# Optimization experiments

Measured on AMD Instinct MI355X. Metric: run time of the kernel, lower is better.

The kernel has to match this reference:

```python
import jax, jax.numpy as jnp
import numpy as np

B, S = 4, 1024
VD, TD, HD = 1024, 768, 2048
NH = 16
HDIM = HD // NH
SCALE = HDIM ** -0.5
THRESH = 2.0 / 3.0


def bitnet_linear(x, w, b):
    # BitNet b1.58 eval-mode: per-tensor abs-mean scale, clamp, ternarize, dense matmul
    scale = jnp.clip(jnp.mean(jnp.abs(w)), 1e-5, 1000.0)
    wn = jnp.clip(w / scale, -10.0, 10.0)
    q = jnp.where(wn > THRESH, 1.0, jnp.where(wn < -THRESH, -1.0, 0.0))
    return x @ (q * scale).T + b


def layernorm(x, g, b, eps=1e-5):
    mu = jnp.mean(x, axis=-1, keepdims=True)
    var = jnp.mean(jnp.square(x - mu), axis=-1, keepdims=True)
    return (x - mu) * jax.lax.rsqrt(var + eps) * g + b


def setup_inputs() -> dict:
    key = jax.random.key(0)
    ks = jax.random.split(key, 8)
    return {
        "vision_features": jax.random.normal(ks[0], (B, VD), jnp.float32),
        "text_features": jax.random.normal(ks[1], (B, S, TD), jnp.float32),
        "text_mask": jnp.ones((B, S), dtype=bool),
        "w_vision_proj": jax.random.normal(ks[2], (HD, VD), jnp.float32),
        "b_vision_proj": jnp.zeros((HD,), jnp.float32),
        "w_text_proj": jax.random.normal(ks[3], (HD, TD), jnp.float32),
        "b_text_proj": jnp.zeros((HD,), jnp.float32),
        "w_text_qkv": jax.random.normal(ks[4], (3 * HD, HD), jnp.float32),
        "b_text_qkv": jnp.zeros((3 * HD,), jnp.float32),
        "ln_text_g": jnp.ones((HD,), jnp.float32),
        "ln_text_b": jnp.zeros((HD,), jnp.float32),
        "w_out": jax.random.normal(ks[5], (HD, HD), jnp.float32),
        "b_out": jnp.zeros((HD,), jnp.float32),
        "ln_cross_g": jnp.ones((HD,), jnp.float32),
        "ln_cross_b": jnp.zeros((HD,), jnp.float32),
    }


def reference(vision_features, text_features, text_mask,
              w_vision_proj, b_vision_proj, w_text_proj, b_text_proj,
              w_text_qkv, b_text_qkv, ln_text_g, ln_text_b,
              w_out, b_out, ln_cross_g, ln_cross_b):
    # projections into shared hidden space (BitNet ternary linears)
    vp = bitnet_linear(vision_features, w_vision_proj, b_vision_proj)        # [B, HD]
    tp = bitnet_linear(text_features, w_text_proj, b_text_proj)              # [B, S, HD]

    # --- text self-attention (no rel-pos bias: the rel-pos branch raises and is swallowed) ---
    tn = layernorm(tp, ln_text_g, ln_text_b)
    qkv = bitnet_linear(tn, w_text_qkv, b_text_qkv)                          # [B, S, 3*HD]
    qkv = qkv.reshape(B, S, 3, NH, HDIM).transpose(2, 0, 3, 1, 4)            # [3, B, H, S, hd]
    tq, tk, tv = qkv[0], qkv[1], qkv[2]
    attn = jnp.einsum('bhqd,bhkd->bhqk', tq, tk) * SCALE                     # [B, H, S, S]
    attn = jnp.where(text_mask[:, None, None, :], attn, -1e9)
    attn = jax.nn.softmax(attn, axis=-1)
    text_self = jnp.einsum('bhqk,bhkd->bhqd', attn, tv)
    text_self = text_self.transpose(0, 2, 1, 3).reshape(B, S, HD)
    text_self = tp + text_self                                               # residual (dropout=id in eval)

    # --- image-to-text attention ---
    # original repeats the single vision query over seq then means the (identical)
    # outputs; mathematically equal to a single-query attention.
    vq = vp.reshape(B, NH, 1, HDIM)                                          # [B, H, 1, hd]
    tk2 = text_self.reshape(B, S, NH, HDIM).transpose(0, 2, 1, 3)            # [B, H, S, hd]
    i2t = jnp.einsum('bhqd,bhkd->bhqk', vq, tk2) * SCALE                     # [B, H, 1, S]
    i2t = jnp.where(text_mask[:, None, None, :], i2t, -1e9)
    i2t = jax.nn.softmax(i2t, axis=-1)
    i2t_out = jnp.einsum('bhqk,bhkd->bhqd', i2t, tk2).reshape(B, HD)         # [B, HD]

    # --- text-to-image attention (single kv "token" per head -> softmax over size-1 axis) ---
    tq2 = text_self.reshape(B, S, NH, HDIM).transpose(0, 2, 1, 3)            # [B, H, S, hd]
    vk = vp.reshape(B, NH, 1, HDIM)                                          # [B, H, 1, hd]
    t2i = jnp.einsum('bhqd,bhkd->bhqk', tq2, vk) * SCALE                     # [B, H, S, 1]
    t2i = jax.nn.softmax(t2i, axis=-1)                                       # all ones (size-1 axis)
    t2i_out = jnp.einsum('bhqk,bhkd->bhqd', t2i, vk)                         # [B, H, S, hd]
    t2i_out = t2i_out.transpose(0, 2, 1, 3).reshape(B, S, HD)

    # --- fusion: shared BitNet output projection + cross norm (inferred continuation) ---
    fused_vision = layernorm(vp + bitnet_linear(i2t_out, w_out, b_out), ln_cross_g, ln_cross_b)
    fused_text = layernorm(text_self + bitnet_linear(t2i_out, w_out, b_out), ln_cross_g, ln_cross_b)
    return fused_vision, fused_text
```

## Files before the change

### kernel.cpp

```cpp
#include <hip/hip_runtime.h>


typedef unsigned short u16;
typedef unsigned int   u32;
typedef __attribute__((ext_vector_type(4))) float f32x4;
typedef __attribute__((ext_vector_type(8))) short short8;
typedef _Float16 half8 __attribute__((ext_vector_type(8)));

__device__ __forceinline__ u16 f2h(float x) {
    _Float16 h = (_Float16)x;
    return __builtin_bit_cast(u16, h);
}
__device__ __forceinline__ f32x4 mfmah(short8 a, short8 b, f32x4 c) {
    return __builtin_amdgcn_mfma_f32_16x16x32_f16(
        __builtin_bit_cast(half8, a), __builtin_bit_cast(half8, b), c, 0, 0, 0);
}
__device__ __forceinline__ void gload16(const void* g, void* l) {
    __builtin_amdgcn_global_load_lds((const __attribute__((address_space(1))) u32*)g,
                                     (__attribute__((address_space(3))) u32*)l, 16, 0, 0);
}

__device__ __forceinline__ float blockReduceSum256(float v, float* red) {
#pragma unroll
    for (int o = 32; o; o >>= 1) v += __shfl_down(v, o);
    int lane = threadIdx.x & 63, w = threadIdx.x >> 6;
    __syncthreads();
    if (lane == 0) red[w] = v;
    __syncthreads();
    return red[0] + red[1] + red[2] + red[3];
}

__global__ __launch_bounds__(256) void k_absmean4(const float* __restrict__ w0, const float* __restrict__ w1,
                                                  const float* __restrict__ w2, const float* __restrict__ w3,
                                                  int n40, int n41, int n42, int n43,
                                                  double* __restrict__ part) {
    int slot = blockIdx.x >> 8, b = blockIdx.x & 255;
    const float* w = (slot == 0) ? w0 : (slot == 1) ? w1 : (slot == 2) ? w2 : w3;
    int n4 = (slot == 0) ? n40 : (slot == 1) ? n41 : (slot == 2) ? n42 : n43;
    const float4* w4 = (const float4*)w;
    double s = 0.0;
    for (int i = b * 256 + threadIdx.x; i < n4; i += 65536) {
        float4 v = w4[i];
        s += (double)fabsf(v.x) + (double)fabsf(v.y) + (double)fabsf(v.z) + (double)fabsf(v.w);
    }
#pragma unroll
    for (int o = 32; o; o >>= 1) s += __shfl_down(s, o);
    __shared__ double p4[4];
    int lane = threadIdx.x & 63, w_ = threadIdx.x >> 6;
    if (lane == 0) p4[w_] = s;
    __syncthreads();
    if (threadIdx.x == 0) part[slot * 256 + b] = p4[0] + p4[1] + p4[2] + p4[3];
}

__global__ void k_finalize(const double* __restrict__ part, float* __restrict__ scf) {
    int w = threadIdx.x >> 6, lane = threadIdx.x & 63;
    double s = 0.0;
    for (int j = lane; j < 256; j += 64) s += part[w * 256 + j];
#pragma unroll
    for (int o = 32; o; o >>= 1) s += __shfl_down(s, o);
    if (lane == 0) {
        const double ns[4] = {2097152.0, 1572864.0, 12582912.0, 4194304.0};
        float v = (float)(s / ns[w]);
        v = fminf(fmaxf(v, 1e-5f), 1000.0f);
        scf[w] = v;
    }
}

__global__ __launch_bounds__(256) void k_quant(const float* __restrict__ w, u32* __restrict__ qd,
                                               int n2, const float* __restrict__ scf, int slot) {
    float s = scf[slot];
    const float th = 2.0f / 3.0f;
    for (int i = blockIdx.x * blockDim.x + threadIdx.x; i < n2; i += gridDim.x * blockDim.x) {
        float2 v = ((const float2*)w)[i];
        float wn0 = v.x / s, wn1 = v.y / s;
        u32 q0 = (wn0 > th) ? 0x3C00u : ((wn0 < -th) ? 0xBC00u : 0u);
        u32 q1 = (wn1 > th) ? 0x3C00u : ((wn1 < -th) ? 0xBC00u : 0u);
        qd[i] = q0 | (q1 << 16);
    }
}

__global__ __launch_bounds__(256) void k_tofp16(const float* __restrict__ x, u32* __restrict__ xs, int n2) {
    for (int i = blockIdx.x * blockDim.x + threadIdx.x; i < n2; i += gridDim.x * blockDim.x) {
        float2 v = ((const float2*)x)[i];
        xs[i] = (u32)f2h(v.x) | (((u32)f2h(v.y)) << 16);
    }
}

__global__ __launch_bounds__(256) void k_gemm(const u16* __restrict__ A, const u16* __restrict__ Bw,
                                              int K, int N, int NB_N,
                                              const float* __restrict__ scf, int slot,
                                              const float* __restrict__ bias,
                                              float* Cf, u16* Cp, int epi) {
    __shared__ __align__(16) u16 ldsA[2][128 * 64];
    __shared__ __align__(16) u16 ldsB[2][128 * 64];
    int m0 = (blockIdx.x / NB_N) * 128;
    int n0 = (blockIdx.x % NB_N) * 128;
    int t = threadIdx.x, lane = t & 63, w = t >> 6;
    int wm = (w >> 1) * 64, wn = (w & 1) * 64;
    f32x4 acc[4][4];
#pragma unroll
    for (int i = 0; i < 4; i++)
#pragma unroll
        for (int j = 0; j < 4; j++) acc[i][j] = (f32x4)(0.0f);

    auto STAGE = [&](int buf, int k0) {
#pragma unroll
        for (int i = 0; i < 4; i++) {
            int c = i * 256 + t;
            int row = c & 127, kg = c >> 7;
            const u16* ga = A + (size_t)(m0 + row) * K + (k0 + kg * 8);
            const u16* gb = Bw + (size_t)(n0 + row) * K + (k0 + kg * 8);
            int db = (i * 256 + w * 64) * 8;
            gload16(ga, ldsA[buf] + db);
            gload16(gb, ldsB[buf] + db);
        }
    };
    auto COMPUTE = [&](int buf) {
#pragma unroll
        for (int kk = 0; kk < 64; kk += 32) {
            int kg4 = (kk >> 3) + (lane >> 4);
            short8 av[4], bv[4];
#pragma unroll
            for (int mi = 0; mi < 4; mi++)
                av[mi] = *(const short8*)(ldsA[buf] + (size_t)(kg4 * 128 + wm + mi * 16 + (lane & 15)) * 8);
#pragma unroll
            for (int ni = 0; ni < 4; ni++)
                bv[ni] = *(const short8*)(ldsB[buf] + (size_t)(kg4 * 128 + wn + ni * 16 + (lane & 15)) * 8);
#pragma unroll
            for (int mi = 0; mi < 4; mi++)
#pragma unroll
                for (int ni = 0; ni < 4; ni++)
                    acc[mi][ni] = mfmah(av[mi], bv[ni], acc[mi][ni]);
        }
    };

    STAGE(0, 0);
    __syncthreads();
    int cur = 0;
    for (int k0 = 64; k0 < K; k0 += 64) {
        STAGE(cur ^ 1, k0);
        COMPUTE(cur);
        __syncthreads();
        cur ^= 1;
    }
    COMPUTE(cur);

    float s = scf[slot];
#pragma unroll
    for (int ni = 0; ni < 4; ni++) {
        int col = n0 + wn + ni * 16 + (lane & 15);
        float bv = bias[col];
#pragma unroll
        for (int mi = 0; mi < 4; mi++) {
            int rb = m0 + wm + mi * 16 + ((lane >> 4) << 2);
#pragma unroll
            for (int j = 0; j < 4; j++) {
                float y = acc[mi][ni][j] * s + bv;
                if (epi == 0) {
                    Cf[(size_t)(rb + j) * N + col] = y;
                } else {
                    Cp[(size_t)(rb + j) * N + col] = f2h(y);
                }
            }
        }
    }
}

__global__ __launch_bounds__(256) void k_vp(const float* __restrict__ vf, const float* __restrict__ w,
                                            const float* __restrict__ bias, const float* __restrict__ scf,
                                            float* __restrict__ vp) {
    __shared__ float xl[4096];
    int t = threadIdx.x;
#pragma unroll
    for (int i = 0; i < 16; i++) xl[t + i * 256] = vf[t + i * 256];
    __syncthreads();
    int lane = t & 63;
    int n = blockIdx.x * 4 + (t >> 6);
    float s = scf[0];
    const float th = 2.0f / 3.0f;
    float a0 = 0, a1 = 0, a2 = 0, a3 = 0;
    const float* wr = w + (size_t)n * 1024;
    for (int k = lane; k < 1024; k += 64) {
        float wn = wr[k] / s;
        float q = (wn > th) ? 1.0f : ((wn < -th) ? -1.0f : 0.0f);
        a0 += xl[k] * q; a1 += xl[1024 + k] * q; a2 += xl[2048 + k] * q; a3 += xl[3072 + k] * q;
    }
#pragma unroll
    for (int o = 32; o; o >>= 1) {
        a0 += __shfl_down(a0, o); a1 += __shfl_down(a1, o);
        a2 += __shfl_down(a2, o); a3 += __shfl_down(a3, o);
    }
    if (lane == 0) {
        float bv = bias[n];
        vp[n] = a0 * s + bv; vp[2048 + n] = a1 * s + bv;
        vp[4096 + n] = a2 * s + bv; vp[6144 + n] = a3 * s + bv;
    }
}

__global__ __launch_bounds__(256) void k_ln1(const float* __restrict__ x, const float* __restrict__ g,
                                             const float* __restrict__ b, u16* __restrict__ tn) {
    __shared__ float red[4];
    int r = blockIdx.x, t = threadIdx.x;
    const float* xr = x + (size_t)r * 2048;
    float v[8]; float s = 0;
#pragma unroll
    for (int i = 0; i < 8; i++) { v[i] = xr[t + i * 256]; s += v[i]; }
    s = blockReduceSum256(s, red);
    float mu = s * (1.0f / 2048.0f);
    float s2 = 0;
#pragma unroll
    for (int i = 0; i < 8; i++) { float d = v[i] - mu; s2 += d * d; }
    s2 = blockReduceSum256(s2, red);
    float rstd = 1.0f / sqrtf(s2 * (1.0f / 2048.0f) + 1e-5f);
#pragma unroll
    for (int i = 0; i < 8; i++) {
        int c = t + i * 256;
        float y = (v[i] - mu) * rstd * g[c] + b[c];
        tn[(size_t)r * 2048 + c] = f2h(y);
    }
}

__global__ __launch_bounds__(256) void k_attn(const u16* __restrict__ qkv, float* ts) {
    __shared__ __align__(16) u16 kp[8192];
    __shared__ __align__(16) u16 vt[128 * 72];
    int t = threadIdx.x, lane = t & 63, w = t >> 6;
    int bh = blockIdx.x >> 4, qb = blockIdx.x & 15;
    int b = bh >> 4, h = bh & 15;
    int rowbase = b * 1024;
    int q0 = qb * 64 + w * 16;
    u16* pl = kp + (size_t)w * 16 * 72;

    short8 qh[4];
    {
        int r = rowbase + q0 + (lane & 15);
        const u16* qp = qkv + (size_t)r * 6144 + h * 128 + (lane >> 4) * 8;
#pragma unroll
        for (int c4 = 0; c4 < 4; c4++) qh[c4] = *(const short8*)(qp + c4 * 32);
    }
    float m[4], ld[4];
#pragma unroll
    for (int j = 0; j < 4; j++) { m[j] = -1e30f; ld[j] = 0.0f; }
    f32x4 po[8];
#pragma unroll
    for (int nt = 0; nt < 8; nt++) po[nt] = (f32x4)(0.0f);
    const float SC = 0.08838834764831845f;

    for (int kt = 0; kt < 16; kt++) {
        __syncthreads();
#pragma unroll
        for (int i = 0; i < 4; i++) {
            int c = i * 256 + t;
            int sl = c & 63, dg = c >> 6;
            const u16* gk = qkv + (size_t)(rowbase + kt * 64 + sl) * 6144 + (2048 + h * 128 + dg * 8);
            gload16(gk, kp + (size_t)(i * 256 + w * 64) * 8);
        }
#pragma unroll
        for (int i = 0; i < 4; i++) {
            int c = i * 256 + t;
            int sl = c & 63, dg = c >> 6;
            const u16* gv = qkv + (size_t)(rowbase + kt * 64 + sl) * 6144 + (4096 + h * 128 + dg * 8);
            short8 vv = *(const short8*)gv;
#pragma unroll
            for (int j = 0; j < 8; j++) vt[(size_t)(dg * 8 + j) * 72 + sl] = (u16)vv[j];
        }
        __syncthreads();

        f32x4 sacc[4];
#pragma unroll
        for (int nt = 0; nt < 4; nt++) sacc[nt] = (f32x4)(0.0f);
#pragma unroll
        for (int c4 = 0; c4 < 4; c4++) {
            int kg = c4 * 4 + (lane >> 4);
#pragma unroll
            for (int nt = 0; nt < 4; nt++) {
                short8 kf = *(const short8*)(kp + (size_t)(kg * 64 + nt * 16 + (lane & 15)) * 8);
                sacc[nt] = mfmah(qh[c4], kf, sacc[nt]);
            }
        }
        float fsc[4], rs[4];
#pragma unroll
        for (int j = 0; j < 4; j++) {
            float mx = fmaxf(fmaxf(sacc[0][j], sacc[1][j]), fmaxf(sacc[2][j], sacc[3][j]));
            mx = fmaxf(mx, __shfl_xor(mx, 1));
            mx = fmaxf(mx, __shfl_xor(mx, 2));
            mx = fmaxf(mx, __shfl_xor(mx, 4));
            mx = fmaxf(mx, __shfl_xor(mx, 8));
            float mn = fmaxf(m[j], mx * SC);
            fsc[j] = expf(m[j] - mn);
            m[j] = mn; rs[j] = 0.0f;
        }
        __syncthreads();
#pragma unroll
        for (int nt = 0; nt < 4; nt++) {
#pragma unroll
            for (int j = 0; j < 4; j++) {
                float p = expf(sacc[nt][j] * SC - m[j]);
                rs[j] += p;
                pl[(size_t)((lane >> 4) * 4 + j) * 72 + nt * 16 + (lane & 15)] = f2h(p);
            }
        }
#pragma unroll
        for (int j = 0; j < 4; j++) {
            float r = rs[j];
            r += __shfl_xor(r, 1); r += __shfl_xor(r, 2);
            r += __shfl_xor(r, 4); r += __shfl_xor(r, 8);
            ld[j] = ld[j] * fsc[j] + r;
        }
#pragma unroll
        for (int nt = 0; nt < 8; nt++)
#pragma unroll
            for (int j = 0; j < 4; j++) po[nt][j] *= fsc[j];

#pragma unroll
        for (int kk2 = 0; kk2 < 2; kk2++) {
            short8 pa = *(const short8*)(pl + (size_t)(lane & 15) * 72 + kk2 * 32 + (lane >> 4) * 8);
#pragma unroll
            for (int nt = 0; nt < 8; nt++) {
                short8 vf = *(const short8*)(vt + (size_t)(nt * 16 + (lane & 15)) * 72 + kk2 * 32 + (lane >> 4) * 8);
                po[nt] = mfmah(pa, vf, po[nt]);
            }
        }
    }
#pragma unroll
    for (int nt = 0; nt < 8; nt++) {
        int d = nt * 16 + (lane & 15);
#pragma unroll
        for (int j = 0; j < 4; j++) {
            int r = rowbase + q0 + (lane >> 4) * 4 + j;
            size_t idx = (size_t)r * 2048 + h * 128 + d;
            ts[idx] = ts[idx] + po[nt][j] / ld[j];
        }
    }
}

__global__ __launch_bounds__(256) void k_i2t(const float* __restrict__ vp, const float* __restrict__ ts,
                                             float* __restrict__ io) {
    __shared__ float vq[128];
    __shared__ float sc[1024];
    __shared__ float red[4];
    __shared__ float part[256];
    int bh = blockIdx.x; int b = bh >> 4, h = bh & 15;
    int t = threadIdx.x, lane = t & 63, w = t >> 6;
    if (t < 128) vq[t] = vp[b * 2048 + h * 128 + t];
    __syncthreads();
    const float SC = 0.08838834764831845f;
    for (int s = w; s < 1024; s += 4) {
        const float* row = ts + (size_t)(b * 1024 + s) * 2048 + h * 128;
        float d = vq[lane] * row[lane] + vq[lane + 64] * row[lane + 64];
#pragma unroll
        for (int o = 32; o; o >>= 1) d += __shfl_down(d, o);
        if (lane == 0) sc[s] = d * SC;
    }
    __syncthreads();
    float mx = -1e30f;
    for (int s = t; s < 1024; s += 256) mx = fmaxf(mx, sc[s]);
#pragma unroll
    for (int o = 32; o; o >>= 1) mx = fmaxf(mx, __shfl_down(mx, o));
    if (lane == 0) red[w] = mx;
    __syncthreads();
    mx = fmaxf(fmaxf(red[0], red[1]), fmaxf(red[2], red[3]));
    __syncthreads();
    float sm = 0;
    for (int s = t; s < 1024; s += 256) { float p = expf(sc[s] - mx); sc[s] = p; sm += p; }
#pragma unroll
    for (int o = 32; o; o >>= 1) sm += __shfl_down(sm, o);
    if (lane == 0) red[w] = sm;
    __syncthreads();
    sm = red[0] + red[1] + red[2] + red[3];
    {
        int d = t & 127, sh = t >> 7;
        float acc = 0;
        const float* base = ts + (size_t)(b * 1024) * 2048 + h * 128 + d;
        for (int s = sh * 512; s < (sh + 1) * 512; s++) acc += sc[s] * base[(size_t)s * 2048];
        part[t] = acc;
    }
    __syncthreads();
    if (t < 128) io[b * 2048 + h * 128 + t] = (part[t] + part[128 + t]) / sm;
}

__global__ __launch_bounds__(256) void k_wout8(const float* __restrict__ i2t, const float* __restrict__ vp,
                                               const float* __restrict__ w, const float* __restrict__ bias,
                                               const float* __restrict__ scf, float* __restrict__ y8) {
    __shared__ float xl[8 * 2048];
    int t = threadIdx.x;
    for (int i = t; i < 16384; i += 256) {
        int rr = i >> 11, cc = i & 2047;
        xl[i] = (rr < 4) ? i2t[rr * 2048 + cc] : vp[(rr - 4) * 2048 + cc];
    }
    __syncthreads();
    int lane = t & 63;
    int n = blockIdx.x * 4 + (t >> 6);
    float s = scf[3];
    const float th = 2.0f / 3.0f;
    float a[8];
#pragma unroll
    for (int i = 0; i < 8; i++) a[i] = 0.0f;
    const float* wr = w + (size_t)n * 2048;
    for (int k = lane; k < 2048; k += 64) {
        float wn = wr[k] / s;
        float q = (wn > th) ? 1.0f : ((wn < -th) ? -1.0f : 0.0f);
#pragma unroll
        for (int i = 0; i < 8; i++) a[i] += xl[i * 2048 + k] * q;
    }
#pragma unroll
    for (int i = 0; i < 8; i++) {
#pragma unroll
        for (int o = 32; o; o >>= 1) a[i] += __shfl_down(a[i], o);
    }
    if (lane == 0) {
        float bv = bias[n];
#pragma unroll
        for (int i = 0; i < 8; i++) y8[i * 2048 + n] = a[i] * s + bv;
    }
}

__global__ __launch_bounds__(256) void k_fln(const float* __restrict__ xa, const float* __restrict__ y8,
                                             const float* __restrict__ g, const float* __restrict__ bb,
                                             float* __restrict__ out, int textmode) {
    __shared__ float red[4];
    int r = blockIdx.x, t = threadIdx.x;
    const float* a = xa + (size_t)r * 2048;
    const float* c = y8 + (size_t)(textmode ? (4 + (r >> 10)) : r) * 2048;
    float v[8]; float s = 0;
#pragma unroll
    for (int i = 0; i < 8; i++) { int cc = t + i * 256; v[i] = a[cc] + c[cc]; s += v[i]; }
    s = blockReduceSum256(s, red);
    float mu = s * (1.0f / 2048.0f);
    float s2 = 0;
#pragma unroll
    for (int i = 0; i < 8; i++) { float d = v[i] - mu; s2 += d * d; }
    s2 = blockReduceSum256(s2, red);
    float rstd = 1.0f / sqrtf(s2 * (1.0f / 2048.0f) + 1e-5f);
#pragma unroll
    for (int i = 0; i < 8; i++) {
        int cc = t + i * 256;
        out[(size_t)r * 2048 + cc] = (v[i] - mu) * rstd * g[cc] + bb[cc];
    }
}

extern "C" void kernel_launch(void* const* d_in, const int* in_sizes, int n_in,
                              void* d_out, int out_size, void* d_ws, size_t ws_size,
                              hipStream_t stream) {
    const float* vf    = (const float*)d_in[0];
    const float* tf    = (const float*)d_in[1];
    const float* w_vp  = (const float*)d_in[3];
    const float* b_vp  = (const float*)d_in[4];
    const float* w_tp  = (const float*)d_in[5];
    const float* b_tp  = (const float*)d_in[6];
    const float* w_qkv = (const float*)d_in[7];
    const float* b_qkv = (const float*)d_in[8];
    const float* lng   = (const float*)d_in[9];
    const float* lnb   = (const float*)d_in[10];
    const float* w_o   = (const float*)d_in[11];
    const float* b_o   = (const float*)d_in[12];
    const float* lcg   = (const float*)d_in[13];
    const float* lcb   = (const float*)d_in[14];
    float* out = (float*)d_out;
    char* ws = (char*)d_ws;

    constexpr size_t OFF_PART  = 0;
    constexpr size_t OFF_SCF   = 49152;
    constexpr size_t OFF_QDTP  = 65536;
    constexpr size_t OFF_QDQKV = 3276800;
    constexpr size_t OFF_XS    = 28442624;
    constexpr size_t OFF_TP    = 34734080;
    constexpr size_t OFF_TN    = 68288512;
    constexpr size_t OFF_QKV   = 85065728;
    constexpr size_t OFF_VP    = 135397376;
    constexpr size_t OFF_I2T   = 135430144;
    constexpr size_t OFF_Y8    = 135462912;

    double* part  = (double*)(ws + OFF_PART);
    float*  scf   = (float*)(ws + OFF_SCF);
    u16*   qd_tp  = (u16*)(ws + OFF_QDTP);
    u16*   qd_qkv = (u16*)(ws + OFF_QDQKV);
    u16*   xs     = (u16*)(ws + OFF_XS);
    float* tpb    = (float*)(ws + OFF_TP);
    u16*   tn     = (u16*)(ws + OFF_TN);
    u16*   qkvp   = (u16*)(ws + OFF_QKV);
    float* vpb    = (float*)(ws + OFF_VP);
    float* i2t    = (float*)(ws + OFF_I2T);
    float* y8     = (float*)(ws + OFF_Y8);

    k_absmean4<<<1024, 256, 0, stream>>>(w_vp, w_tp, w_qkv, w_o,
                                         2048 * 1024 / 4, 2048 * 768 / 4,
                                         6144 * 2048 / 4, 2048 * 2048 / 4, part);
    k_finalize<<<1, 256, 0, stream>>>(part, scf);

    k_quant<<<2048, 256, 0, stream>>>(w_tp,  (u32*)qd_tp,  2048 * 768  / 2, scf, 1);
    k_quant<<<4096, 256, 0, stream>>>(w_qkv, (u32*)qd_qkv, 6144 * 2048 / 2, scf, 2);
    k_tofp16<<<2048, 256, 0, stream>>>(tf, (u32*)xs, 4096 * 768 / 2);

    k_gemm<<<512, 256, 0, stream>>>(xs, qd_tp, 768, 2048, 16, scf, 1, b_tp, tpb, nullptr, 0);
    k_vp<<<512, 256, 0, stream>>>(vf, w_vp, b_vp, scf, vpb);

    k_ln1<<<4096, 256, 0, stream>>>(tpb, lng, lnb, tn);

    k_gemm<<<1536, 256, 0, stream>>>(tn, qd_qkv, 2048, 6144, 48, scf, 2, b_qkv, nullptr, qkvp, 1);

    k_attn<<<1024, 256, 0, stream>>>(qkvp, tpb);

    k_i2t<<<64, 256, 0, stream>>>(vpb, tpb, i2t);

    k_wout8<<<512, 256, 0, stream>>>(i2t, vpb, w_o, b_o, scf, y8);

    k_fln<<<4, 256, 0, stream>>>(vpb, y8, lcg, lcb, out, 0);
    k_fln<<<4096, 256, 0, stream>>>(tpb, y8, lcg, lcb, out + 8192, 1);
    (void)in_sizes; (void)n_in; (void)out_size; (void)ws_size;
}
```

Measured before the change: 677.3 us.

## Merge quant launches, single-buffer GEMM with grouped tile order, double query tiles in attention

```diff
diff --git a/kernel.cpp b/kernel.cpp
--- a/kernel.cpp
+++ b/kernel.cpp
@@ -66,11 +66,18 @@
     }
 }
 
-__global__ __launch_bounds__(256) void k_quant(const float* __restrict__ w, u32* __restrict__ qd,
-                                               int n2, const float* __restrict__ scf, int slot) {
-    float s = scf[slot];
+__global__ __launch_bounds__(256) void k_quant2(const float* __restrict__ wa, u32* __restrict__ qa, int n2a,
+                                                const float* __restrict__ wb, u32* __restrict__ qb, int n2b,
+                                                const float* __restrict__ scf) {
+    int seg = (blockIdx.x >= 1024) ? 1 : 0;
+    const float* w = seg ? wb : wa;
+    u32* qd = seg ? qb : qa;
+    int n2 = seg ? n2b : n2a;
+    float s = scf[seg ? 2 : 1];
+    int b = seg ? (blockIdx.x - 1024) : blockIdx.x;
+    int nb = seg ? (gridDim.x - 1024) : 1024;
     const float th = 2.0f / 3.0f;
-    for (int i = blockIdx.x * blockDim.x + threadIdx.x; i < n2; i += gridDim.x * blockDim.x) {
+    for (int i = b * 256 + threadIdx.x; i < n2; i += nb * 256) {
         float2 v = ((const float2*)w)[i];
         float wn0 = v.x / s, wn1 = v.y / s;
         u32 q0 = (wn0 > th) ? 0x3C00u : ((wn0 < -th) ? 0xBC00u : 0u);
@@ -91,10 +98,13 @@
                                               const float* __restrict__ scf, int slot,
                                               const float* __restrict__ bias,
                                               float* Cf, u16* Cp, int epi) {
-    __shared__ __align__(16) u16 ldsA[2][128 * 64];
-    __shared__ __align__(16) u16 ldsB[2][128 * 64];
-    int m0 = (blockIdx.x / NB_N) * 128;
-    int n0 = (blockIdx.x % NB_N) * 128;
+    __shared__ __align__(16) u16 ldsA[128 * 64];
+    __shared__ __align__(16) u16 ldsB[128 * 64];
+    int id = blockIdx.x;
+    int r8 = id >> 3;
+    int nn = r8 % NB_N;
+    int mm = (r8 / NB_N) * 8 + (id & 7);
+    int m0 = mm * 128, n0 = nn * 128;
     int t = threadIdx.x, lane = t & 63, w = t >> 6;
     int wm = (w >> 1) * 64, wn = (w & 1) * 64;
     f32x4 acc[4][4];
@@ -103,7 +113,8 @@
 #pragma unroll
         for (int j = 0; j < 4; j++) acc[i][j] = (f32x4)(0.0f);
 
-    auto STAGE = [&](int buf, int k0) {
+    for (int k0 = 0; k0 < K; k0 += 64) {
+        __syncthreads();
 #pragma unroll
         for (int i = 0; i < 4; i++) {
             int c = i * 256 + t;
@@ -111,40 +122,27 @@
             const u16* ga = A + (size_t)(m0 + row) * K + (k0 + kg * 8);
             const u16* gb = Bw + (size_t)(n0 + row) * K + (k0 + kg * 8);
             int db = (i * 256 + w * 64) * 8;
-            gload16(ga, ldsA[buf] + db);
-            gload16(gb, ldsB[buf] + db);
-        }
-    };
-    auto COMPUTE = [&](int buf) {
+            gload16(ga, ldsA + db);
+            gload16(gb, ldsB + db);
+        }
+        __syncthreads();
 #pragma unroll
         for (int kk = 0; kk < 64; kk += 32) {
             int kg4 = (kk >> 3) + (lane >> 4);
             short8 av[4], bv[4];
 #pragma unroll
             for (int mi = 0; mi < 4; mi++)
-                av[mi] = *(const short8*)(ldsA[buf] + (size_t)(kg4 * 128 + wm + mi * 16 + (lane & 15)) * 8);
+                av[mi] = *(const short8*)(ldsA + (size_t)(kg4 * 128 + wm + mi * 16 + (lane & 15)) * 8);
 #pragma unroll
             for (int ni = 0; ni < 4; ni++)
-                bv[ni] = *(const short8*)(ldsB[buf] + (size_t)(kg4 * 128 + wn + ni * 16 + (lane & 15)) * 8);
+                bv[ni] = *(const short8*)(ldsB + (size_t)(kg4 * 128 + wn + ni * 16 + (lane & 15)) * 8);
 #pragma unroll
             for (int mi = 0; mi < 4; mi++)
 #pragma unroll
                 for (int ni = 0; ni < 4; ni++)
                     acc[mi][ni] = mfmah(av[mi], bv[ni], acc[mi][ni]);
         }
-    };
-
-    STAGE(0, 0);
-    __syncthreads();
-    int cur = 0;
-    for (int k0 = 64; k0 < K; k0 += 64) {
-        STAGE(cur ^ 1, k0);
-        COMPUTE(cur);
-        __syncthreads();
-        cur ^= 1;
-    }
-    COMPUTE(cur);
-
+    }
     float s = scf[slot];
 #pragma unroll
     for (int ni = 0; ni < 4; ni++) {
@@ -224,25 +222,31 @@
     __shared__ __align__(16) u16 kp[8192];
     __shared__ __align__(16) u16 vt[128 * 72];
     int t = threadIdx.x, lane = t & 63, w = t >> 6;
-    int bh = blockIdx.x >> 4, qb = blockIdx.x & 15;
+    int id = blockIdx.x;
+    int bh = ((id >> 6) << 3) | (id & 7);
+    int qsuper = (id >> 3) & 7;
     int b = bh >> 4, h = bh & 15;
     int rowbase = b * 1024;
-    int q0 = qb * 64 + w * 16;
     u16* pl = kp + (size_t)w * 16 * 72;
 
-    short8 qh[4];
-    {
-        int r = rowbase + q0 + (lane & 15);
+    short8 qh[2][4];
+#pragma unroll
+    for (int qt = 0; qt < 2; qt++) {
+        int r = rowbase + qsuper * 128 + qt * 64 + w * 16 + (lane & 15);
         const u16* qp = qkv + (size_t)r * 6144 + h * 128 + (lane >> 4) * 8;
 #pragma unroll
-        for (int c4 = 0; c4 < 4; c4++) qh[c4] = *(const short8*)(qp + c4 * 32);
-    }
-    float m[4], ld[4];
-#pragma unroll
-    for (int j = 0; j < 4; j++) { m[j] = -1e30f; ld[j] = 0.0f; }
-    f32x4 po[8];
-#pragma unroll
-    for (int nt = 0; nt < 8; nt++) po[nt] = (f32x4)(0.0f);
+        for (int c4 = 0; c4 < 4; c4++) qh[qt][c4] = *(const short8*)(qp + c4 * 32);
+    }
+    float m[2][4], ld[2][4];
+#pragma unroll
+    for (int qt = 0; qt < 2; qt++)
+#pragma unroll
+        for (int j = 0; j < 4; j++) { m[qt][j] = -1e30f; ld[qt][j] = 0.0f; }
+    f32x4 po[2][8];
+#pragma unroll
+    for (int qt = 0; qt < 2; qt++)
+#pragma unroll
+        for (int nt = 0; nt < 8; nt++) po[qt][nt] = (f32x4)(0.0f);
     const float SC = 0.08838834764831845f;
 
     for (int kt = 0; kt < 16; kt++) {
@@ -265,72 +269,84 @@
         }
         __syncthreads();
 
-        f32x4 sacc[4];
-#pragma unroll
-        for (int nt = 0; nt < 4; nt++) sacc[nt] = (f32x4)(0.0f);
+        f32x4 sacc[2][4];
+#pragma unroll
+        for (int qt = 0; qt < 2; qt++)
+#pragma unroll
+            for (int nt = 0; nt < 4; nt++) sacc[qt][nt] = (f32x4)(0.0f);
 #pragma unroll
         for (int c4 = 0; c4 < 4; c4++) {
             int kg = c4 * 4 + (lane >> 4);
 #pragma unroll
             for (int nt = 0; nt < 4; nt++) {
                 short8 kf = *(const short8*)(kp + (size_t)(kg * 64 + nt * 16 + (lane & 15)) * 8);
-                sacc[nt] = mfmah(qh[c4], kf, sacc[nt]);
-            }
-        }
-        float fsc[4], rs[4];
-#pragma unroll
-        for (int j = 0; j < 4; j++) {
-            float mx = fmaxf(fmaxf(sacc[0][j], sacc[1][j]), fmaxf(sacc[2][j], sacc[3][j]));
-            mx = fmaxf(mx, __shfl_xor(mx, 1));
-            mx = fmaxf(mx, __shfl_xor(mx, 2));
-            mx = fmaxf(mx, __shfl_xor(mx, 4));
-            mx = fmaxf(mx, __shfl_xor(mx, 8));
-            float mn = fmaxf(m[j], mx * SC);
-            fsc[j] = expf(m[j] - mn);
-            m[j] = mn; rs[j] = 0.0f;
-        }
+                sacc[0][nt] = mfmah(qh[0][c4], kf, sacc[0][nt]);
+                sacc[1][nt] = mfmah(qh[1][c4], kf, sacc[1][nt]);
+            }
+        }
+        float fsc[2][4];
+#pragma unroll
+        for (int qt = 0; qt < 2; qt++)
+#pragma unroll
+            for (int j = 0; j < 4; j++) {
+                float mx = fmaxf(fmaxf(sacc[qt][0][j], sacc[qt][1][j]),
+                                 fmaxf(sacc[qt][2][j], sacc[qt][3][j]));
+                mx = fmaxf(mx, __shfl_xor(mx, 1));
+                mx = fmaxf(mx, __shfl_xor(mx, 2));
+                mx = fmaxf(mx, __shfl_xor(mx, 4));
+                mx = fmaxf(mx, __shfl_xor(mx, 8));
+                float mn = fmaxf(m[qt][j], mx * SC);
+                fsc[qt][j] = expf(m[qt][j] - mn);
+                m[qt][j] = mn;
+            }
         __syncthreads();
 #pragma unroll
-        for (int nt = 0; nt < 4; nt++) {
+        for (int qt = 0; qt < 2; qt++) {
+            float rs[4] = {0.0f, 0.0f, 0.0f, 0.0f};
+#pragma unroll
+            for (int nt = 0; nt < 4; nt++) {
+#pragma unroll
+                for (int j = 0; j < 4; j++) {
+                    float p = expf(sacc[qt][nt][j] * SC - m[qt][j]);
+                    rs[j] += p;
+                    pl[(size_t)((lane >> 4) * 4 + j) * 72 + nt * 16 + (lane & 15)] = f2h(p);
+                }
+            }
 #pragma unroll
             for (int j = 0; j < 4; j++) {
-                float p = expf(sacc[nt][j] * SC - m[j]);
-                rs[j] += p;
-                pl[(size_t)((lane >> 4) * 4 + j) * 72 + nt * 16 + (lane & 15)] = f2h(p);
-            }
-        }
-#pragma unroll
-        for (int j = 0; j < 4; j++) {
-            float r = rs[j];
-            r += __shfl_xor(r, 1); r += __shfl_xor(r, 2);
-            r += __shfl_xor(r, 4); r += __shfl_xor(r, 8);
-            ld[j] = ld[j] * fsc[j] + r;
-        }
-#pragma unroll
-        for (int nt = 0; nt < 8; nt++)
-#pragma unroll
-            for (int j = 0; j < 4; j++) po[nt][j] *= fsc[j];
-
-#pragma unroll
-        for (int kk2 = 0; kk2 < 2; kk2++) {
-            short8 pa = *(const short8*)(pl + (size_t)(lane & 15) * 72 + kk2 * 32 + (lane >> 4) * 8);
-#pragma unroll
-            for (int nt = 0; nt < 8; nt++) {
-                short8 vf = *(const short8*)(vt + (size_t)(nt * 16 + (lane & 15)) * 72 + kk2 * 32 + (lane >> 4) * 8);
-                po[nt] = mfmah(pa, vf, po[nt]);
-            }
-        }
-    }
-#pragma unroll
-    for (int nt = 0; nt < 8; nt++) {
-        int d = nt * 16 + (lane & 15);
-#pragma unroll
-        for (int j = 0; j < 4; j++) {
-            int r = rowbase + q0 + (lane >> 4) * 4 + j;
-            size_t idx = (size_t)r * 2048 + h * 128 + d;
-            ts[idx] = ts[idx] + po[nt][j] / ld[j];
-        }
-    }
+                float r = rs[j];
+                r += __shfl_xor(r, 1); r += __shfl_xor(r, 2);
+                r += __shfl_xor(r, 4); r += __shfl_xor(r, 8);
+                ld[qt][j] = ld[qt][j] * fsc[qt][j] + r;
+            }
+#pragma unroll
+            for (int nt = 0; nt < 8; nt++)
+#pragma unroll
+                for (int j = 0; j < 4; j++) po[qt][nt][j] *= fsc[qt][j];
+
+#pragma unroll
+            for (int kk2 = 0; kk2 < 2; kk2++) {
+                short8 pa = *(const short8*)(pl + (size_t)(lane & 15) * 72 + kk2 * 32 + (lane >> 4) * 8);
+#pragma unroll
+                for (int nt = 0; nt < 8; nt++) {
+                    short8 vf = *(const short8*)(vt + (size_t)(nt * 16 + (lane & 15)) * 72 + kk2 * 32 + (lane >> 4) * 8);
+                    po[qt][nt] = mfmah(pa, vf, po[qt][nt]);
+                }
+            }
+        }
+    }
+#pragma unroll
+    for (int qt = 0; qt < 2; qt++)
+#pragma unroll
+        for (int nt = 0; nt < 8; nt++) {
+            int d = nt * 16 + (lane & 15);
+#pragma unroll
+            for (int j = 0; j < 4; j++) {
+                int r = rowbase + qsuper * 128 + qt * 64 + w * 16 + (lane >> 4) * 4 + j;
+                size_t idx = (size_t)r * 2048 + h * 128 + d;
+                ts[idx] = ts[idx] + po[qt][nt][j] / ld[qt][j];
+            }
+        }
 }
 
 __global__ __launch_bounds__(256) void k_i2t(const float* __restrict__ vp, const float* __restrict__ ts,
@@ -487,8 +503,8 @@
                                          6144 * 2048 / 4, 2048 * 2048 / 4, part);
     k_finalize<<<1, 256, 0, stream>>>(part, scf);
 
-    k_quant<<<2048, 256, 0, stream>>>(w_tp,  (u32*)qd_tp,  2048 * 768  / 2, scf, 1);
-    k_quant<<<4096, 256, 0, stream>>>(w_qkv, (u32*)qd_qkv, 6144 * 2048 / 2, scf, 2);
+    k_quant2<<<5120, 256, 0, stream>>>(w_tp, (u32*)qd_tp, 2048 * 768 / 2,
+                                       w_qkv, (u32*)qd_qkv, 6144 * 2048 / 2, scf);
     k_tofp16<<<2048, 256, 0, stream>>>(tf, (u32*)xs, 4096 * 768 / 2);
 
     k_gemm<<<512, 256, 0, stream>>>(xs, qd_tp, 768, 2048, 16, scf, 1, b_tp, tpb, nullptr, 0);
@@ -498,7 +514,7 @@
 
     k_gemm<<<1536, 256, 0, stream>>>(tn, qd_qkv, 2048, 6144, 48, scf, 2, b_qkv, nullptr, qkvp, 1);
 
-    k_attn<<<1024, 256, 0, stream>>>(qkvp, tpb);
+    k_attn<<<512, 256, 0, stream>>>(qkvp, tpb);
 
     k_i2t<<<64, 256, 0, stream>>>(vpb, tpb, i2t);
 
```

New measurement: 709.6 us. +4.8%, slower.
